# Kernel tuning notes

Measured on AMD Instinct MI355X. Metric: run time of the kernel, lower is better.

Reference implementation:

```python
import jax, jax.numpy as jnp
import numpy as np

NEG_SLOPE = 0.2


def gat_layer(x, src, dst, W, a_src, a_dst, b, heads, ch):
    """PyG-style GATConv (self-loops already appended to src/dst)."""
    N = x.shape[0]
    h = (x @ W).reshape(N, heads, ch)                 # [N,H,C]
    alpha_s = (h * a_src).sum(-1)                      # [N,H]
    alpha_d = (h * a_dst).sum(-1)                      # [N,H]
    e = jax.nn.leaky_relu(alpha_s[src] + alpha_d[dst], NEG_SLOPE)  # [E,H]
    # segment softmax over edges grouped by destination node
    m = jax.ops.segment_max(e, dst, num_segments=N)    # [N,H]
    ex = jnp.exp(e - m[dst])
    s = jax.ops.segment_sum(ex, dst, num_segments=N)   # [N,H]
    a = ex / (s[dst] + 1e-16)                          # [E,H]
    out = jax.ops.segment_sum(h[src] * a[:, :, None], dst, num_segments=N)  # [N,H,C]
    return out.reshape(N, heads * ch) + b


def setup_inputs() -> dict:
    key = jax.random.key(0)
    ks = jax.random.split(key, 12)
    N, E = 20000, 320000
    IN, HID, HEADS, OUT = 3, 64, 4, 21
    x = jax.random.normal(ks[0], (N, IN), dtype=jnp.float32)
    edge_index = jax.random.randint(ks[1], (2, E), 0, N, dtype=jnp.int32)
    g = 1.0 / np.sqrt(HID)
    inp = {
        "x": x,
        "edge_index": edge_index,
        "W1": jax.random.normal(ks[2], (IN, HEADS * HID), dtype=jnp.float32) * (1.0 / np.sqrt(IN)),
        "att_src1": jax.random.normal(ks[3], (HEADS, HID), dtype=jnp.float32) * g,
        "att_dst1": jax.random.normal(ks[4], (HEADS, HID), dtype=jnp.float32) * g,
        "b1": jnp.zeros((HEADS * HID,), dtype=jnp.float32),
        "W2": jax.random.normal(ks[5], (HEADS * HID, OUT), dtype=jnp.float32) * (1.0 / np.sqrt(HEADS * HID)),
        "att_src2": jax.random.normal(ks[6], (1, OUT), dtype=jnp.float32) * (1.0 / np.sqrt(OUT)),
        "att_dst2": jax.random.normal(ks[7], (1, OUT), dtype=jnp.float32) * (1.0 / np.sqrt(OUT)),
        "b2": jnp.zeros((OUT,), dtype=jnp.float32),
    }
    return inp


def reference(x, edge_index, W1, att_src1, att_dst1, b1, W2, att_src2, att_dst2, b2):
    N = x.shape[0]
    loop = jnp.arange(N, dtype=edge_index.dtype)
    src = jnp.concatenate([edge_index[0], loop])
    dst = jnp.concatenate([edge_index[1], loop])
    h = gat_layer(x, src, dst, W1, att_src1, att_dst1, b1, heads=4, ch=64)
    h = jax.nn.relu(h)
    h = gat_layer(h, src, dst, W2, att_src2, att_dst2, b2, heads=1, ch=21)
    return jax.nn.softmax(h, axis=1)
```

## Files before the change

kernel.cpp:

```cpp
#include <hip/hip_runtime.h>

#define HID   256
#define HEADS 4
#define OUT_C 21
#define H2S   24
#define NEG_SLOPE 0.2f
#define CAP   96


__global__ void alpha_zero_kernel(const float* __restrict__ x, const float* __restrict__ W1,
                                  const float* __restrict__ a_s, const float* __restrict__ a_d,
                                  float4* __restrict__ pxs, float4* __restrict__ ad1,
                                  int* __restrict__ cursor, int N) {
    __shared__ float wa[24];
    int t = threadIdx.x;
    int head = t >> 6;
    float avs = a_s[t], avd = a_d[t];
#pragma unroll
    for (int k = 0; k < 3; ++k) {
        float w = W1[k * HID + t];
        float ps = w * avs, pd = w * avd;
        for (int m = 32; m >= 1; m >>= 1) {
            ps += __shfl_xor(ps, m);
            pd += __shfl_xor(pd, m);
        }
        if ((t & 63) == 0) {
            wa[k * HEADS + head] = ps;
            wa[12 + k * HEADS + head] = pd;
        }
    }
    __syncthreads();
    int n = blockIdx.x * 256 + t;
    if (n >= N) return;
    cursor[n] = 0;
    float x0 = x[n * 3], x1 = x[n * 3 + 1], x2 = x[n * 3 + 2];
    float s[HEADS], d[HEADS];
#pragma unroll
    for (int h = 0; h < HEADS; ++h) {
        s[h] = x0 * wa[h] + x1 * wa[4 + h] + x2 * wa[8 + h];
        d[h] = x0 * wa[12 + h] + x1 * wa[16 + h] + x2 * wa[20 + h];
    }
    pxs[2 * n]     = make_float4(x0, x1, x2, s[0]);
    pxs[2 * n + 1] = make_float4(s[1], s[2], s[3], 0.f);
    ad1[n] = make_float4(d[0], d[1], d[2], d[3]);
}


__global__ void scatter_count_kernel(const int* __restrict__ ei, int E, int N,
                                     int* __restrict__ cursor, int* __restrict__ table) {
    int i = blockIdx.x * blockDim.x + threadIdx.x;
    if (i >= E + N) return;
    int src, dst;
    if (i < E) { src = ei[i]; dst = ei[E + i]; }
    else       { src = dst = i - E; }
    int pos = atomicAdd(&cursor[dst], 1);
    if (pos < CAP) table[dst * CAP + pos] = src;
}


__global__ void aggr_node_kernel(const int* __restrict__ cursor, const int* __restrict__ table,
                                 const float4* __restrict__ pxs, const float4* __restrict__ ad1,
                                 const float* __restrict__ W1, const float* __restrict__ b1,
                                 const float* __restrict__ W2, const float* __restrict__ a2s,
                                 const float* __restrict__ a2d, float* __restrict__ h2p,
                                 int N) {
    __shared__ float4 wc[HID];
    __shared__ float  w2s[HID * H2S];
    int tid = threadIdx.x;
    {
        int k = tid;
        wc[k] = make_float4(W1[k], W1[HID + k], W1[2 * HID + k], b1[k]);
        for (int idx = tid; idx < HID * OUT_C; idx += 256) {
            int k2 = idx / OUT_C;
            int o = idx - k2 * OUT_C;
            w2s[k2 * H2S + o] = W2[idx];
        }
    }
    __syncthreads();
    int g = blockIdx.x * 256 + tid;
    int n = g >> 3;
    int sub = g & 7;
    if (n >= N) return;

    float4 adv = ad1[n];
    float ad[HEADS] = {adv.x, adv.y, adv.z, adv.w};
    float sum[HEADS] = {0, 0, 0, 0};
    float s0[HEADS] = {0, 0, 0, 0}, s1[HEADS] = {0, 0, 0, 0}, s2[HEADS] = {0, 0, 0, 0};
    int deg = min(cursor[n], CAP);
    const int* row = table + (size_t)n * CAP;
    int j = sub;
    int s_next = row[j < deg ? j : 0];
    float4 A_next = pxs[2 * s_next];
    float4 B_next = pxs[2 * s_next + 1];
    while (j < deg) {
        float4 A = A_next, B = B_next;
        int jn = j + 8;
        s_next = row[jn < deg ? jn : 0];
        A_next = pxs[2 * s_next];
        B_next = pxs[2 * s_next + 1];
        float a[HEADS] = {A.w, B.x, B.y, B.z};
#pragma unroll
        for (int h = 0; h < HEADS; ++h) {
            float e = a[h] + ad[h];
            e = (e > 0.f) ? e : NEG_SLOPE * e;
            float p = __expf(e);
            sum[h] += p;
            s0[h] = fmaf(p, A.x, s0[h]);
            s1[h] = fmaf(p, A.y, s1[h]);
            s2[h] = fmaf(p, A.z, s2[h]);
        }
        j = jn;
    }
#pragma unroll
    for (int h = 0; h < HEADS; ++h) {
        s0[h] += __shfl_xor(s0[h], 1);  s0[h] += __shfl_xor(s0[h], 2);  s0[h] += __shfl_xor(s0[h], 4);
        s1[h] += __shfl_xor(s1[h], 1);  s1[h] += __shfl_xor(s1[h], 2);  s1[h] += __shfl_xor(s1[h], 4);
        s2[h] += __shfl_xor(s2[h], 1);  s2[h] += __shfl_xor(s2[h], 2);  s2[h] += __shfl_xor(s2[h], 4);
        sum[h] += __shfl_xor(sum[h], 1); sum[h] += __shfl_xor(sum[h], 2); sum[h] += __shfl_xor(sum[h], 4);
    }

    float acc[OUT_C];
#pragma unroll
    for (int o = 0; o < OUT_C; ++o) acc[o] = 0.f;
#pragma unroll
    for (int h = 0; h < HEADS; ++h) {
        float gx = s0[h], gy = s1[h], gz = s2[h];
        float gi = 1.0f / (sum[h] + 1e-16f);
#pragma unroll
        for (int i2 = 0; i2 < 8; ++i2) {
            int k = h * 64 + i2 * 8 + sub;
            float4 w = wc[k];
            float r = fmaf(fmaf(gx, w.x, fmaf(gy, w.y, gz * w.z)), gi, w.w);
            r = fmaxf(r, 0.f);
            const float4* wr = (const float4*)&w2s[k * H2S];
            float4 w0 = wr[0], w1 = wr[1], w2v = wr[2], w3 = wr[3], w4 = wr[4], w5 = wr[5];
            acc[0]  = fmaf(r, w0.x, acc[0]);   acc[1]  = fmaf(r, w0.y, acc[1]);
            acc[2]  = fmaf(r, w0.z, acc[2]);   acc[3]  = fmaf(r, w0.w, acc[3]);
            acc[4]  = fmaf(r, w1.x, acc[4]);   acc[5]  = fmaf(r, w1.y, acc[5]);
            acc[6]  = fmaf(r, w1.z, acc[6]);   acc[7]  = fmaf(r, w1.w, acc[7]);
            acc[8]  = fmaf(r, w2v.x, acc[8]);  acc[9]  = fmaf(r, w2v.y, acc[9]);
            acc[10] = fmaf(r, w2v.z, acc[10]); acc[11] = fmaf(r, w2v.w, acc[11]);
            acc[12] = fmaf(r, w3.x, acc[12]);  acc[13] = fmaf(r, w3.y, acc[13]);
            acc[14] = fmaf(r, w3.z, acc[14]);  acc[15] = fmaf(r, w3.w, acc[15]);
            acc[16] = fmaf(r, w4.x, acc[16]);  acc[17] = fmaf(r, w4.y, acc[17]);
            acc[18] = fmaf(r, w4.z, acc[18]);  acc[19] = fmaf(r, w4.w, acc[19]);
            acc[20] = fmaf(r, w5.x, acc[20]);
        }
    }
#pragma unroll
    for (int o = 0; o < OUT_C; ++o) {
        acc[o] += __shfl_xor(acc[o], 1);
        acc[o] += __shfl_xor(acc[o], 2);
        acc[o] += __shfl_xor(acc[o], 4);
    }
    if (sub == 0) {
        float s = 0.f, d = 0.f;
#pragma unroll
        for (int o = 0; o < OUT_C; ++o) {
            s = fmaf(acc[o], a2s[o], s);
            d = fmaf(acc[o], a2d[o], d);
        }
        float4* hv = (float4*)&h2p[n * H2S];
        hv[0] = make_float4(acc[0], acc[1], acc[2], acc[3]);
        hv[1] = make_float4(acc[4], acc[5], acc[6], acc[7]);
        hv[2] = make_float4(acc[8], acc[9], acc[10], acc[11]);
        hv[3] = make_float4(acc[12], acc[13], acc[14], acc[15]);
        hv[4] = make_float4(acc[16], acc[17], acc[18], acc[19]);
        hv[5] = make_float4(acc[20], s, d, 0.f);
    }
}


__global__ void l2_aggr_kernel(const int* __restrict__ cursor, const int* __restrict__ table,
                               const float* __restrict__ h2p, const float* __restrict__ b2,
                               float* __restrict__ out, int N) {
    int wave = threadIdx.x >> 6;
    int lane = threadIdx.x & 63;
    int n = blockIdx.x * 4 + wave;
    if (n >= N) return;
    int grp = lane / 21;
    int c = lane - grp * 21;
    bool ingrp = (grp < 3);
    int deg = min(cursor[n], CAP);
    const int* row = table + (size_t)n * CAP;
    int iters = (deg + 2) / 3;
    float ad = h2p[n * H2S + 22];

    int j = grp;
    bool v0 = ingrp && (j < deg);
    int s0 = row[v0 ? j : 0];
    float a0 = h2p[s0 * H2S + 21];
    float vv0 = h2p[s0 * H2S + c];
    j += 3;
    bool v1 = ingrp && (j < deg);
    int s1 = row[v1 ? j : 0];

    float accv = 0.f, sump = 0.f;
    for (int it = 0; it < iters; ++it) {
        float a1 = h2p[s1 * H2S + 21];
        float vv1 = h2p[s1 * H2S + c];
        j += 3;
        bool v2 = ingrp && (j < deg);
        int s2 = row[v2 ? j : 0];
        float e = a0 + ad;
        e = (e > 0.f) ? e : NEG_SLOPE * e;
        float p = v0 ? __expf(e) : 0.f;
        sump += p;
        accv = fmaf(p, vv0, accv);
        a0 = a1; vv0 = vv1; v0 = v1; v1 = v2; s1 = s2;
    }
    float acc_t = accv + __shfl(accv, lane + 21) + __shfl(accv, lane + 42);
    float sum_t = __shfl(sump, 0) + __shfl(sump, 21) + __shfl(sump, 42);
    float o = (lane < OUT_C) ? (acc_t / (sum_t + 1e-16f) + b2[lane]) : -1e30f;
    float mx = o;
    for (int m = 16; m >= 1; m >>= 1) mx = fmaxf(mx, __shfl_xor(mx, m));
    float ex = (lane < OUT_C) ? __expf(o - mx) : 0.f;
    float tot = ex;
    for (int m = 16; m >= 1; m >>= 1) tot += __shfl_xor(tot, m);
    if (lane < OUT_C) out[n * OUT_C + lane] = ex / tot;
}


extern "C" void kernel_launch(void* const* d_in, const int* in_sizes, int n_in,
                              void* d_out, int out_size, void* d_ws, size_t ws_size,
                              hipStream_t stream) {
    const float* x     = (const float*)d_in[0];
    const int*   ei    = (const int*)d_in[1];
    const float* W1    = (const float*)d_in[2];
    const float* asrc1 = (const float*)d_in[3];
    const float* adst1 = (const float*)d_in[4];
    const float* b1    = (const float*)d_in[5];
    const float* W2    = (const float*)d_in[6];
    const float* asrc2 = (const float*)d_in[7];
    const float* adst2 = (const float*)d_in[8];
    const float* b2    = (const float*)d_in[9];
    float* out = (float*)d_out;

    const int N = in_sizes[0] / 3;
    const int E = in_sizes[1] / 2;
    const int ET = E + N;

    size_t off = 0;
    auto alloc = [&](size_t bytes) -> char* {
        off = (off + 255) & ~(size_t)255;
        char* p = (char*)d_ws + off;
        off += bytes;
        return p;
    };
    int*    cursor = (int*)alloc((size_t)N * 4);
    int*    table  = (int*)alloc((size_t)N * CAP * 4);
    float4* pxs    = (float4*)alloc((size_t)N * 32);
    float4* ad1    = (float4*)alloc((size_t)N * 16);
    float*  h2p    = (float*)alloc((size_t)N * H2S * 4);
    (void)ws_size;

    alpha_zero_kernel<<<(N + 255) / 256, 256, 0, stream>>>(x, W1, asrc1, adst1,
                                                           pxs, ad1, cursor, N);
    scatter_count_kernel<<<(ET + 255) / 256, 256, 0, stream>>>(ei, E, N, cursor, table);

    aggr_node_kernel<<<(8 * N + 255) / 256, 256, 0, stream>>>(cursor, table, pxs, ad1,
                                                              W1, b1, W2, asrc2, adst2,
                                                              h2p, N);
    l2_aggr_kernel<<<(N + 3) / 4, 256, 0, stream>>>(cursor, table, h2p, b2, out, N);
}
```

Measured before the change: 129.8 us.

## Shrink adjacency cap, vectorize edge scatter, split layer-2 aggregation across two waves

Reduces the per-node neighbor table capacity from 96 to 64 and uses shift indexing, shrinking the workspace footprint. The scatter kernel now loads edge pairs as int2 so each thread handles two edges. The layer-2 aggregation spreads each node across two waves (six groups) and combines their partials through shared memory, and one float4 shared-memory load is replaced by a scalar load. The smaller cap risks silently dropping neighbors for high-degree nodes; with about 17 average in-degree this is unlikely but not guaranteed.

```diff
diff --git a/kernel.cpp b/kernel.cpp
--- a/kernel.cpp
+++ b/kernel.cpp
@@ -5,7 +5,8 @@
 #define OUT_C 21
 #define H2S   24
 #define NEG_SLOPE 0.2f
-#define CAP   96
+#define CAP   64
+#define CAPSH 6
 
 
 __global__ void alpha_zero_kernel(const float* __restrict__ x, const float* __restrict__ W1,
@@ -49,12 +50,25 @@
 __global__ void scatter_count_kernel(const int* __restrict__ ei, int E, int N,
                                      int* __restrict__ cursor, int* __restrict__ table) {
     int i = blockIdx.x * blockDim.x + threadIdx.x;
-    if (i >= E + N) return;
-    int src, dst;
-    if (i < E) { src = ei[i]; dst = ei[E + i]; }
-    else       { src = dst = i - E; }
-    int pos = atomicAdd(&cursor[dst], 1);
-    if (pos < CAP) table[dst * CAP + pos] = src;
+    int Eh = E >> 1;
+    if (i < Eh) {
+        int2 s2 = ((const int2*)ei)[i];
+        int2 d2 = ((const int2*)(ei + E))[i];
+        int p0 = atomicAdd(&cursor[d2.x], 1);
+        if (p0 < CAP) table[(d2.x << CAPSH) + p0] = s2.x;
+        int p1 = atomicAdd(&cursor[d2.y], 1);
+        if (p1 < CAP) table[(d2.y << CAPSH) + p1] = s2.y;
+    } else {
+        int n = i - Eh;
+        if (n < N) {
+            int p = atomicAdd(&cursor[n], 1);
+            if (p < CAP) table[(n << CAPSH) + p] = n;
+        } else if ((E & 1) && n == N) {
+            int src = ei[E - 1], dst = ei[2 * E - 1];
+            int p = atomicAdd(&cursor[dst], 1);
+            if (p < CAP) table[(dst << CAPSH) + p] = src;
+        }
+    }
 }
 
 
@@ -87,7 +101,7 @@
     float sum[HEADS] = {0, 0, 0, 0};
     float s0[HEADS] = {0, 0, 0, 0}, s1[HEADS] = {0, 0, 0, 0}, s2[HEADS] = {0, 0, 0, 0};
     int deg = min(cursor[n], CAP);
-    const int* row = table + (size_t)n * CAP;
+    const int* row = table + ((size_t)n << CAPSH);
     int j = sub;
     int s_next = row[j < deg ? j : 0];
     float4 A_next = pxs[2 * s_next];
@@ -133,7 +147,8 @@
             float r = fmaf(fmaf(gx, w.x, fmaf(gy, w.y, gz * w.z)), gi, w.w);
             r = fmaxf(r, 0.f);
             const float4* wr = (const float4*)&w2s[k * H2S];
-            float4 w0 = wr[0], w1 = wr[1], w2v = wr[2], w3 = wr[3], w4 = wr[4], w5 = wr[5];
+            float4 w0 = wr[0], w1 = wr[1], w2v = wr[2], w3 = wr[3], w4 = wr[4];
+            float w20 = w2s[k * H2S + 20];
             acc[0]  = fmaf(r, w0.x, acc[0]);   acc[1]  = fmaf(r, w0.y, acc[1]);
             acc[2]  = fmaf(r, w0.z, acc[2]);   acc[3]  = fmaf(r, w0.w, acc[3]);
             acc[4]  = fmaf(r, w1.x, acc[4]);   acc[5]  = fmaf(r, w1.y, acc[5]);
@@ -144,7 +159,7 @@
             acc[14] = fmaf(r, w3.z, acc[14]);  acc[15] = fmaf(r, w3.w, acc[15]);
             acc[16] = fmaf(r, w4.x, acc[16]);  acc[17] = fmaf(r, w4.y, acc[17]);
             acc[18] = fmaf(r, w4.z, acc[18]);  acc[19] = fmaf(r, w4.w, acc[19]);
-            acc[20] = fmaf(r, w5.x, acc[20]);
+            acc[20] = fmaf(r, w20, acc[20]);
         }
     }
 #pragma unroll
@@ -174,50 +189,64 @@
 __global__ void l2_aggr_kernel(const int* __restrict__ cursor, const int* __restrict__ table,
                                const float* __restrict__ h2p, const float* __restrict__ b2,
                                float* __restrict__ out, int N) {
-    int wave = threadIdx.x >> 6;
-    int lane = threadIdx.x & 63;
-    int n = blockIdx.x * 4 + wave;
-    if (n >= N) return;
-    int grp = lane / 21;
-    int c = lane - grp * 21;
-    bool ingrp = (grp < 3);
-    int deg = min(cursor[n], CAP);
-    const int* row = table + (size_t)n * CAP;
-    int iters = (deg + 2) / 3;
-    float ad = h2p[n * H2S + 22];
+    __shared__ float part[2][44];
+    int tid = threadIdx.x;
+    int wave = tid >> 6;
+    int lane = tid & 63;
+    int slot = wave >> 1;
+    int w2 = wave & 1;
+    int n = blockIdx.x * 2 + slot;
+    bool an = (n < N);
+    int nn = an ? n : 0;
+
+    int lgrp = lane / 21;
+    int c = lane - lgrp * 21;
+    bool ingrp = (lgrp < 3) && an;
+    int grp = w2 * 3 + lgrp;
+    int deg = an ? min(cursor[nn], CAP) : 0;
+    const int* row = table + ((size_t)nn << CAPSH);
+    float ad = h2p[nn * H2S + 22];
 
     int j = grp;
     bool v0 = ingrp && (j < deg);
-    int s0 = row[v0 ? j : 0];
-    float a0 = h2p[s0 * H2S + 21];
-    float vv0 = h2p[s0 * H2S + c];
-    j += 3;
+    int si0 = row[v0 ? j : 0];
+    float a0 = h2p[si0 * H2S + 21];
+    float vv0 = h2p[si0 * H2S + c];
+    j += 6;
     bool v1 = ingrp && (j < deg);
-    int s1 = row[v1 ? j : 0];
+    int si1 = row[v1 ? j : 0];
 
     float accv = 0.f, sump = 0.f;
+    int iters = (deg + 5) / 6;
     for (int it = 0; it < iters; ++it) {
-        float a1 = h2p[s1 * H2S + 21];
-        float vv1 = h2p[s1 * H2S + c];
-        j += 3;
+        float a1 = h2p[si1 * H2S + 21];
+        float vv1 = h2p[si1 * H2S + c];
+        j += 6;
         bool v2 = ingrp && (j < deg);
-        int s2 = row[v2 ? j : 0];
+        int si2 = row[v2 ? j : 0];
         float e = a0 + ad;
         e = (e > 0.f) ? e : NEG_SLOPE * e;
         float p = v0 ? __expf(e) : 0.f;
         sump += p;
         accv = fmaf(p, vv0, accv);
-        a0 = a1; vv0 = vv1; v0 = v1; v1 = v2; s1 = s2;
+        a0 = a1; vv0 = vv1; v0 = v1; v1 = v2; si1 = si2;
     }
     float acc_t = accv + __shfl(accv, lane + 21) + __shfl(accv, lane + 42);
     float sum_t = __shfl(sump, 0) + __shfl(sump, 21) + __shfl(sump, 42);
-    float o = (lane < OUT_C) ? (acc_t / (sum_t + 1e-16f) + b2[lane]) : -1e30f;
-    float mx = o;
-    for (int m = 16; m >= 1; m >>= 1) mx = fmaxf(mx, __shfl_xor(mx, m));
-    float ex = (lane < OUT_C) ? __expf(o - mx) : 0.f;
-    float tot = ex;
-    for (int m = 16; m >= 1; m >>= 1) tot += __shfl_xor(tot, m);
-    if (lane < OUT_C) out[n * OUT_C + lane] = ex / tot;
+    if (lane < OUT_C) part[slot][w2 * 22 + lane] = acc_t;
+    if (lane == 0)    part[slot][w2 * 22 + 21] = sum_t;
+    __syncthreads();
+    if (w2 == 0) {
+        float accT = (lane < OUT_C) ? (part[slot][lane] + part[slot][22 + lane]) : 0.f;
+        float sumT = part[slot][21] + part[slot][43];
+        float o = (lane < OUT_C) ? (accT / (sumT + 1e-16f) + b2[lane]) : -1e30f;
+        float mx = o;
+        for (int m = 16; m >= 1; m >>= 1) mx = fmaxf(mx, __shfl_xor(mx, m));
+        float ex = (lane < OUT_C) ? __expf(o - mx) : 0.f;
+        float tot = ex;
+        for (int m = 16; m >= 1; m >>= 1) tot += __shfl_xor(tot, m);
+        if (an && lane < OUT_C) out[n * OUT_C + lane] = ex / tot;
+    }
 }
 
 
@@ -238,7 +267,6 @@
 
     const int N = in_sizes[0] / 3;
     const int E = in_sizes[1] / 2;
-    const int ET = E + N;
 
     size_t off = 0;
     auto alloc = [&](size_t bytes) -> char* {
@@ -256,10 +284,11 @@
 
     alpha_zero_kernel<<<(N + 255) / 256, 256, 0, stream>>>(x, W1, asrc1, adst1,
                                                            pxs, ad1, cursor, N);
-    scatter_count_kernel<<<(ET + 255) / 256, 256, 0, stream>>>(ei, E, N, cursor, table);
+    int sthreads = (E >> 1) + N + (E & 1);
+    scatter_count_kernel<<<(sthreads + 255) / 256, 256, 0, stream>>>(ei, E, N, cursor, table);
 
     aggr_node_kernel<<<(8 * N + 255) / 256, 256, 0, stream>>>(cursor, table, pxs, ad1,
                                                               W1, b1, W2, asrc2, adst2,
                                                               h2p, N);
-    l2_aggr_kernel<<<(N + 3) / 4, 256, 0, stream>>>(cursor, table, h2p, b2, out, N);
-}
+    l2_aggr_kernel<<<(N + 1) / 2, 256, 0, stream>>>(cursor, table, h2p, b2, out, N);
+}
```

After: 131.4 us. Within noise of the previous version (+1.3%).
